# Kernel optimization log

Measured on AMD Instinct MI355X. Metric: run time of the kernel, lower is better.

The kernel has to match this reference:

```python
import jax, jax.numpy as jnp
import numpy as np

N = 10000      # nodes
E = 160000     # edges
C = 72         # hidden dim = 18 * mul (mul=4)
A = 16         # node_attr dim (16x0e)
L = 3          # layers
O = 64         # output dim (64x0e)
B = 16         # graphs in batch
IN_DIM = 18    # irreps_node_input dim
SH = 9         # spherical harmonics dim, lmax=2
FC = 100       # radial MLP hidden (fc_neurons=[1,100])
MAX_RADIUS = 2.0
NUM_NEIGHBORS = 16.0
NUM_NODES = 625.0


def sph_harm_l2(d):
    # component-normalized real spherical harmonics up to l=2 on unit vectors d [E,3]
    x, y, z = d[:, 0], d[:, 1], d[:, 2]
    s3, s5, s15 = 3.0 ** 0.5, 5.0 ** 0.5, 15.0 ** 0.5
    return jnp.stack([
        jnp.ones_like(x),
        s3 * x, s3 * y, s3 * z,
        s15 * x * y, s15 * y * z, (s5 / 2.0) * (3.0 * z * z - 1.0),
        s15 * x * z, (s15 / 2.0) * (x * x - y * y),
    ], axis=1)  # [E, 9]


def setup_inputs() -> dict:
    key = jax.random.key(0)
    ks = jax.random.split(key, 16)
    pos = jax.random.normal(ks[0], (N, 3), dtype=jnp.float32)
    node_attr = jax.random.normal(ks[1], (N, A), dtype=jnp.float32)
    batch = jnp.sort(jax.random.randint(ks[2], (N,), 0, B))
    edge_src = jax.random.randint(ks[3], (E,), 0, N)
    edge_dst = jax.random.randint(ks[4], (E,), 0, N)
    W_in = jax.random.normal(ks[5], (IN_DIM, C), dtype=jnp.float32) / np.sqrt(IN_DIM)
    W_tp = jax.random.normal(ks[6], (L, SH, C, C), dtype=jnp.float32) / np.sqrt(C)
    W_self = jax.random.normal(ks[7], (L, C, C), dtype=jnp.float32) / np.sqrt(C)
    W_attr = jax.random.normal(ks[8], (L, A, C), dtype=jnp.float32) / np.sqrt(A)
    fc1_w = jax.random.normal(ks[9], (L, 1, FC), dtype=jnp.float32)
    fc1_b = jnp.zeros((L, FC), dtype=jnp.float32)
    fc2_w = jax.random.normal(ks[10], (L, FC, SH), dtype=jnp.float32) / np.sqrt(FC)
    W_out = jax.random.normal(ks[11], (C, O), dtype=jnp.float32) / np.sqrt(C)
    return {"pos": pos, "node_attr": node_attr, "batch": batch,
            "edge_src": edge_src, "edge_dst": edge_dst,
            "W_in": W_in, "W_tp": W_tp, "W_self": W_self, "W_attr": W_attr,
            "fc1_w": fc1_w, "fc1_b": fc1_b, "fc2_w": fc2_w, "W_out": W_out}


def reference(pos, node_attr, batch, edge_src, edge_dst,
              W_in, W_tp, W_self, W_attr, fc1_w, fc1_b, fc2_w, W_out):
    n = pos.shape[0]
    # edge geometry
    rvec = pos[edge_src] - pos[edge_dst]                      # [E,3]
    r = jnp.linalg.norm(rvec, axis=1, keepdims=True)          # [E,1]
    dvec = rvec / jnp.maximum(r, 1e-9)
    sh = sph_harm_l2(dvec)                                    # [E,9]
    # single cosine radial basis with cutoff at max_radius (number_of_basis=1)
    t = r / MAX_RADIUS
    emb = jnp.where(t < 1.0, jnp.cos(0.5 * jnp.pi * t), 0.0)  # [E,1]
    # node inputs: fixed one-hot on the scalar channel, embedded to hidden dim
    onehot = jnp.zeros((IN_DIM,), dtype=pos.dtype).at[0].set(1.0)
    h = jnp.broadcast_to((onehot @ W_in)[None, :], (n, C))    # [N,C]
    for l in range(L):
        # radial MLP -> per-edge, per-SH-path weights
        u = jax.nn.silu(emb @ fc1_w[l] + fc1_b[l]) @ fc2_w[l]  # [E,9]
        path = u * sh                                          # [E,9]
        hs = h[edge_src]                                       # [E,C]
        m = jnp.zeros_like(hs)
        for s in range(SH):  # fixed small set of tensor-product paths
            m = m + path[:, s:s + 1] * (hs @ W_tp[l, s])       # [E,C]
        agg = jax.ops.segment_sum(m, edge_dst, num_segments=n) / np.sqrt(NUM_NEIGHBORS)
        h = jax.nn.gelu(agg + h @ W_self[l] + node_attr @ W_attr[l])
    out_nodes = h @ W_out                                      # [N,O]
    pooled = jax.ops.segment_sum(out_nodes, batch, num_segments=B)
    return pooled / np.sqrt(NUM_NODES)                         # [B,O]
```

## Files before the change

### kernel.cpp

```cpp
#include <hip/hip_runtime.h>
#include <math.h>

#define NN 10000
#define NE 160000
#define CC 72
#define AA 16
#define LL 3
#define OO 64
#define NBATCH 16
#define SH 9
#define FCN 100
#define KK (SH*CC)
#define KA 736
#define KP 768
#define KG 96
#define NT 5
#define PSTRIDE 12
#define NB 1024

typedef __attribute__((ext_vector_type(8))) short bf16x8;
typedef __attribute__((ext_vector_type(4))) float f32x4;

static __device__ __forceinline__ float gelu_tanh(float x) {
    float x3 = x * x * x;
    float inner = 0.7978845608028654f * (x + 0.044715f * x3);
    return 0.5f * x * (1.0f + tanhf(inner));
}
static __device__ __forceinline__ unsigned short f2bf(float x) {
    unsigned int u = __float_as_uint(x);
    u += 0x7FFFu + ((u >> 16) & 1u);
    return (unsigned short)(u >> 16);
}

__global__ void k_hist(const float* __restrict__ pos, const int* __restrict__ esrc,
                       const int* __restrict__ edst, int* __restrict__ cnt) {
    int e = blockIdx.x * blockDim.x + threadIdx.x;
    if (e >= NE) return;
    int s = esrc[e], d = edst[e];
    float dx = pos[3 * s] - pos[3 * d];
    float dy = pos[3 * s + 1] - pos[3 * d + 1];
    float dz = pos[3 * s + 2] - pos[3 * d + 2];
    float r = sqrtf(dx * dx + dy * dy + dz * dz);
    if (r * 0.5f < 1.0f) atomicAdd(&cnt[d], 1);
}

__global__ void k_scan(const int* __restrict__ cnt, int* __restrict__ off) {
    __shared__ int sa[256], sb[256];
    const int PER = 40;
    int t = threadIdx.x;
    int base = t * PER;
    int loc[PER];
    int run = 0;
#pragma unroll
    for (int i = 0; i < PER; ++i) {
        int idx = base + i;
        int v = (idx < NN) ? cnt[idx] : 0;
        loc[i] = run;
        run += v;
    }
    sa[t] = run;
    __syncthreads();
    int* in = sa; int* out = sb;
    for (int o = 1; o < 256; o <<= 1) {
        int v = in[t];
        if (t >= o) v += in[t - o];
        out[t] = v;
        __syncthreads();
        int* tmp = in; in = out; out = tmp;
    }
    int ebase = (t > 0) ? in[t - 1] : 0;
#pragma unroll
    for (int i = 0; i < PER; ++i) {
        int idx = base + i;
        if (idx <= NN) off[idx] = ebase + loc[i];
    }
}

__global__ void k_scatter2(const float* __restrict__ pos, const int* __restrict__ esrc,
                           const int* __restrict__ edst, const int* __restrict__ off,
                           int* __restrict__ cur, int* __restrict__ src_s,
                           int* __restrict__ dst_s) {
    int e = blockIdx.x * blockDim.x + threadIdx.x;
    if (e >= NE) return;
    int s = esrc[e], d = edst[e];
    float dx = pos[3 * s] - pos[3 * d];
    float dy = pos[3 * s + 1] - pos[3 * d + 1];
    float dz = pos[3 * s + 2] - pos[3 * d + 2];
    float r = sqrtf(dx * dx + dy * dy + dz * dz);
    if (r * 0.5f < 1.0f) {
        int slot = off[d] + atomicAdd(&cur[d], 1);
        src_s[slot] = s;
        dst_s[slot] = d;
    }
}

__global__ void k_utab(const float* __restrict__ fc1w, const float* __restrict__ fc1b,
                       const float* __restrict__ fc2w, float* __restrict__ U) {
    int i = blockIdx.x * blockDim.x + threadIdx.x;
    if (i >= LL * (NB + 1)) return;
    int l = i / (NB + 1), b = i - l * (NB + 1);
    float emb = cosf(1.5707963267948966f * ((float)b / (float)NB));
    float u[SH];
#pragma unroll
    for (int q = 0; q < SH; ++q) u[q] = 0.f;
    const float* w1 = &fc1w[l * FCN];
    const float* b1 = &fc1b[l * FCN];
    const float* w2 = &fc2w[l * FCN * SH];
    for (int f = 0; f < FCN; ++f) {
        float a = emb * w1[f] + b1[f];
        float si = a / (1.0f + expf(-a));
#pragma unroll
        for (int q = 0; q < SH; ++q) u[q] += si * w2[f * SH + q];
    }
    float* ud = &U[(size_t)i * 12];
#pragma unroll
    for (int q = 0; q < SH; ++q) ud[q] = u[q];
    ud[9] = 0.f; ud[10] = 0.f; ud[11] = 0.f;
}

__global__ __launch_bounds__(256) void k_path2(const float* __restrict__ pos,
                                               const int* __restrict__ src_s,
                                               const int* __restrict__ dst_s,
                                               const float* __restrict__ U,
                                               const int* __restrict__ off,
                                               float* __restrict__ path) {
    int slot = blockIdx.x * blockDim.x + threadIdx.x;
    if (slot >= off[NN]) return;
    int s = src_s[slot], d = dst_s[slot];
    float dx = pos[3 * s] - pos[3 * d];
    float dy = pos[3 * s + 1] - pos[3 * d + 1];
    float dz = pos[3 * s + 2] - pos[3 * d + 2];
    float r = sqrtf(dx * dx + dy * dy + dz * dz);
    float inv = 1.0f / fmaxf(r, 1e-9f);
    float x = dx * inv, y = dy * inv, z = dz * inv;
    const float s3 = 1.7320508075688772f;
    const float s5 = 2.23606797749979f;
    const float s15 = 3.872983346207417f;
    float sh[SH];
    sh[0] = 1.0f;
    sh[1] = s3 * x;
    sh[2] = s3 * y;
    sh[3] = s3 * z;
    sh[4] = s15 * x * y;
    sh[5] = s15 * y * z;
    sh[6] = 0.5f * s5 * (3.0f * z * z - 1.0f);
    sh[7] = s15 * x * z;
    sh[8] = 0.5f * s15 * (x * x - y * y);

    float fb = r * 0.5f * (float)NB;
    int b0 = (int)fb;
    float fr = fb - (float)b0;

#pragma unroll
    for (int l = 0; l < LL; ++l) {
        const float* t0 = &U[((size_t)l * (NB + 1) + b0) * 12];
        float4 a0 = *(const float4*)(t0 + 0);
        float4 a1 = *(const float4*)(t0 + 4);
        float  a2 = t0[8];
        float4 c0 = *(const float4*)(t0 + 12);
        float4 c1 = *(const float4*)(t0 + 16);
        float  c2 = t0[20];
        float u0 = a0.x + fr * (c0.x - a0.x);
        float u1 = a0.y + fr * (c0.y - a0.y);
        float u2 = a0.z + fr * (c0.z - a0.z);
        float u3 = a0.w + fr * (c0.w - a0.w);
        float u4 = a1.x + fr * (c1.x - a1.x);
        float u5 = a1.y + fr * (c1.y - a1.y);
        float u6 = a1.z + fr * (c1.z - a1.z);
        float u7 = a1.w + fr * (c1.w - a1.w);
        float u8 = a2   + fr * (c2   - a2);
        float* pd = &path[((size_t)l * NE + slot) * PSTRIDE];
        *(float4*)(pd + 0) = make_float4(u0 * sh[0], u1 * sh[1], u2 * sh[2], u3 * sh[3]);
        *(float4*)(pd + 4) = make_float4(u4 * sh[4], u5 * sh[5], u6 * sh[6], u7 * sh[7]);
        *(float4*)(pd + 8) = make_float4(u8 * sh[8], 0.f, 0.f, 0.f);
    }
}

__global__ void k_init(const float* __restrict__ W_in, float* __restrict__ h) {
    int i = blockIdx.x * blockDim.x + threadIdx.x;
    if (i < NN * CC) h[i] = W_in[i % CC];
}

__global__ void k_wcat2(const float* __restrict__ Wtp, const float* __restrict__ Wself,
                        const float* __restrict__ Wattr, unsigned short* __restrict__ Wb) {
    int i = blockIdx.x * blockDim.x + threadIdx.x;
    if (i >= LL * NT * KG * 128) return;
    int l = i / (NT * KG * 128);
    int rem = i - l * (NT * KG * 128);
    int nt = rem / (KG * 128); rem -= nt * (KG * 128);
    int kg = rem / 128; int e = rem - kg * 128;
    int n = nt * 16 + (e >> 3);
    int k = kg * 8 + (e & 7);
    float v = 0.f;
    if (n < CC && k < KA) {
        if (k < KK)            v = 0.25f * Wtp[(size_t)l * KK * CC + k * CC + n];
        else if (k < KK + CC)  v = Wself[(size_t)l * CC * CC + (k - KK) * CC + n];
        else                   v = Wattr[(size_t)l * AA * CC + (k - KK - CC) * CC + n];
    }
    Wb[i] = f2bf(v);
}

__global__ __launch_bounds__(1024) void k_layer(const float* __restrict__ h,
                                                const float* __restrict__ attr,
                                                const float* __restrict__ path_l,
                                                const int* __restrict__ src_s,
                                                const int* __restrict__ off,
                                                const unsigned short* __restrict__ Wb,
                                                float* __restrict__ hout) {
    __shared__ unsigned short Alds[KG * 128];
    __shared__ float red[3 * NT * 64 * 4];
    int t = threadIdx.x, w = t >> 6, lane = t & 63;
    int n0 = blockIdx.x * 16;
    int d = n0 + w;

    float a1[SH], a2[SH];
#pragma unroll
    for (int q = 0; q < SH; ++q) { a1[q] = 0.f; a2[q] = 0.f; }
    int b = off[d], e = off[d + 1];
    bool two = lane < (CC - 64);
    for (int i = b; i < e; ++i) {
        int s = src_s[i];
        float hv1 = h[(size_t)s * CC + lane];
        float hv2 = two ? h[(size_t)s * CC + 64 + lane] : 0.f;
        const float* p = &path_l[(size_t)i * PSTRIDE];
        float4 p0 = *(const float4*)p;
        float4 p1 = *(const float4*)(p + 4);
        float p8 = p[8];
        a1[0] += p0.x * hv1; a2[0] += p0.x * hv2;
        a1[1] += p0.y * hv1; a2[1] += p0.y * hv2;
        a1[2] += p0.z * hv1; a2[2] += p0.z * hv2;
        a1[3] += p0.w * hv1; a2[3] += p0.w * hv2;
        a1[4] += p1.x * hv1; a2[4] += p1.x * hv2;
        a1[5] += p1.y * hv1; a2[5] += p1.y * hv2;
        a1[6] += p1.z * hv1; a2[6] += p1.z * hv2;
        a1[7] += p1.w * hv1; a2[7] += p1.w * hv2;
        a1[8] += p8 * hv1;   a2[8] += p8 * hv2;
    }
    unsigned short* At = Alds + w * 8;
    int kgc = lane >> 3, kjc = lane & 7;
#pragma unroll
    for (int q = 0; q < SH; ++q) {
        At[(9 * q + kgc) * 128 + kjc] = f2bf(a1[q]);
        if (two) At[(9 * q + 8) * 128 + lane] = f2bf(a2[q]);
    }
    At[(81 + kgc) * 128 + kjc] = f2bf(h[(size_t)d * CC + lane]);
    if (two) At[89 * 128 + lane] = f2bf(h[(size_t)d * CC + 64 + lane]);
    if (lane < AA) At[(90 + (lane >> 3)) * 128 + (lane & 7)] = f2bf(attr[(size_t)d * AA + lane]);
    if (lane < 32) At[(92 + (lane >> 3)) * 128 + (lane & 7)] = 0;
    __syncthreads();

    if (w < 4) {
        const unsigned short* Ab = Alds + (lane & 15) * 8;
        const unsigned short* Bb = Wb + (lane & 15) * 8;
        f32x4 acc[NT];
#pragma unroll
        for (int nt = 0; nt < NT; ++nt) acc[nt] = (f32x4){0.f, 0.f, 0.f, 0.f};
        int s0 = w * 6;
#pragma unroll
        for (int s = 0; s < 6; ++s) {
            int kg = (s0 + s) * 4 + (lane >> 4);
            bf16x8 af = *(const bf16x8*)(Ab + (size_t)kg * 128);
#pragma unroll
            for (int nt = 0; nt < NT; ++nt) {
                bf16x8 bf = *(const bf16x8*)(Bb + ((size_t)nt * KG + kg) * 128);
                acc[nt] = __builtin_amdgcn_mfma_f32_16x16x32_bf16(af, bf, acc[nt], 0, 0, 0);
            }
        }
        if (w) {
#pragma unroll
            for (int nt = 0; nt < NT; ++nt)
                *(f32x4*)&red[(((w - 1) * NT + nt) * 64 + lane) * 4] = acc[nt];
        }
        __syncthreads();
        if (w == 0) {
            int cb = lane & 15, rb = (lane >> 4) * 4;
            int row = n0 + rb;
#pragma unroll
            for (int nt = 0; nt < NT; ++nt) {
                f32x4 p0 = *(const f32x4*)&red[((0 * NT + nt) * 64 + lane) * 4];
                f32x4 p1 = *(const f32x4*)&red[((1 * NT + nt) * 64 + lane) * 4];
                f32x4 p2 = *(const f32x4*)&red[((2 * NT + nt) * 64 + lane) * 4];
                int col = nt * 16 + cb;
                if (col < CC) {
#pragma unroll
                    for (int j = 0; j < 4; ++j) {
                        float v = acc[nt][j] + p0[j] + p1[j] + p2[j];
                        hout[(size_t)(row + j) * CC + col] = gelu_tanh(v);
                    }
                }
            }
        }
    } else {
        __syncthreads();
    }
}

__global__ __launch_bounds__(256) void k_pool(const float* __restrict__ h,
                                              const int* __restrict__ batch,
                                              float* __restrict__ hp) {
    __shared__ float sp[NBATCH * CC];
    int t = threadIdx.x;
    for (int i = t; i < NBATCH * CC; i += 256) sp[i] = 0.f;
    __syncthreads();
    int n0 = blockIdx.x * 16;
    for (int i = t; i < 16 * CC; i += 256) {
        int nl = i / CC, c = i - nl * CC;
        int n = n0 + nl;
        if (n < NN) atomicAdd(&sp[batch[n] * CC + c], h[(size_t)n * CC + c]);
    }
    __syncthreads();
    for (int i = t; i < NBATCH * CC; i += 256) {
        float v = sp[i];
        if (v != 0.f) atomicAdd(&hp[i], v);
    }
}

__global__ __launch_bounds__(1024) void k_outmm(const float* __restrict__ hp,
                                                const float* __restrict__ Wout,
                                                float* __restrict__ out) {
    __shared__ float hs[NBATCH * CC];
    int t = threadIdx.x;
    for (int i = t; i < NBATCH * CC; i += 1024) hs[i] = hp[i];
    __syncthreads();
    int b = t >> 6, o = t & 63;
    float acc = 0.f;
#pragma unroll 8
    for (int c = 0; c < CC; ++c) acc += hs[b * CC + c] * Wout[c * OO + o];
    out[t] = acc * (1.0f / 25.0f);
}

extern "C" void kernel_launch(void* const* d_in, const int* in_sizes, int n_in,
                              void* d_out, int out_size, void* d_ws, size_t ws_size,
                              hipStream_t stream) {
    const float* pos       = (const float*)d_in[0];
    const float* node_attr = (const float*)d_in[1];
    const int*   batch     = (const int*)d_in[2];
    const int*   esrc      = (const int*)d_in[3];
    const int*   edst      = (const int*)d_in[4];
    const float* W_in      = (const float*)d_in[5];
    const float* W_tp      = (const float*)d_in[6];
    const float* W_self    = (const float*)d_in[7];
    const float* W_attr    = (const float*)d_in[8];
    const float* fc1w      = (const float*)d_in[9];
    const float* fc1b      = (const float*)d_in[10];
    const float* fc2w      = (const float*)d_in[11];
    const float* W_out     = (const float*)d_in[12];
    float* out = (float*)d_out;

    char* p = (char*)d_ws;
    auto alloc = [&](size_t bytes) -> void* {
        void* r = (void*)p;
        p += (bytes + 255) & ~(size_t)255;
        return r;
    };
    int*   cnt   = (int*)alloc((size_t)NN * 4);
    int*   cur   = (int*)alloc((size_t)NN * 4);
    int*   off   = (int*)alloc((size_t)(NN + 1) * 4);
    int*   src_s = (int*)alloc((size_t)NE * 4);
    int*   dst_s = (int*)alloc((size_t)NE * 4);
    float* path  = (float*)alloc((size_t)LL * NE * PSTRIDE * 4);
    float* U     = (float*)alloc((size_t)LL * (NB + 1) * 12 * 4);
    unsigned short* Wb = (unsigned short*)alloc((size_t)LL * NT * KG * 128 * 2);
    float* h0    = (float*)alloc((size_t)NN * CC * 4);
    float* h1    = (float*)alloc((size_t)NN * CC * 4);
    float* hp    = (float*)alloc((size_t)NBATCH * CC * 4);

    hipMemsetAsync(cnt, 0, (size_t)NN * 4, stream);
    hipMemsetAsync(cur, 0, (size_t)NN * 4, stream);
    hipMemsetAsync(hp, 0, (size_t)NBATCH * CC * 4, stream);

    k_hist<<<(NE + 255) / 256, 256, 0, stream>>>(pos, esrc, edst, cnt);
    k_utab<<<(LL * (NB + 1) + 255) / 256, 256, 0, stream>>>(fc1w, fc1b, fc2w, U);
    k_wcat2<<<(LL * NT * KG * 128 + 255) / 256, 256, 0, stream>>>(W_tp, W_self, W_attr, Wb);
    k_init<<<(NN * CC + 255) / 256, 256, 0, stream>>>(W_in, h0);
    k_scan<<<1, 256, 0, stream>>>(cnt, off);
    k_scatter2<<<(NE + 255) / 256, 256, 0, stream>>>(pos, esrc, edst, off, cur, src_s, dst_s);
    k_path2<<<(NE + 255) / 256, 256, 0, stream>>>(pos, src_s, dst_s, U, off, path);

    const float* hin = h0;
    float* hout = h1;
    for (int l = 0; l < LL; ++l) {
        k_layer<<<NN / 16, 1024, 0, stream>>>(hin, node_attr,
                                              path + (size_t)l * NE * PSTRIDE, src_s, off,
                                              Wb + (size_t)l * NT * KG * 128, hout);
        const float* tmp = hin; hin = hout; hout = (float*)tmp;
    }
    k_pool<<<(NN + 15) / 16, 256, 0, stream>>>(hin, batch, hp);
    k_outmm<<<1, 1024, 0, stream>>>(hp, W_out, out);
}
```

Measured before the change: 166.0 us.

## Fuse prep kernels, store hidden state in bf16, stage path in LDS, split MFMA by tile

Four setup kernels (histogram, radial table, weight packing, h init) are merged into one launch, and the three memsets are collapsed into one by reordering the workspace. Hidden features are stored as bf16 to halve the gather traffic in each layer. Per-block path coefficients are staged in shared memory with batched source loads. The MFMA stage now assigns one output tile per wave instead of splitting K across waves and reducing through LDS. The bf16 hidden state loses precision across layers, and the EMAX chunk loop adds extra block barriers.

Result: faster. 150.8 us (-9.2%).

```diff
diff --git a/kernel.cpp b/kernel.cpp
--- a/kernel.cpp
+++ b/kernel.cpp
@@ -17,6 +17,7 @@
 #define NT 5
 #define PSTRIDE 12
 #define NB 1024
+#define EMAX 176
 
 typedef __attribute__((ext_vector_type(8))) short bf16x8;
 typedef __attribute__((ext_vector_type(4))) float f32x4;
@@ -31,17 +32,93 @@
     u += 0x7FFFu + ((u >> 16) & 1u);
     return (unsigned short)(u >> 16);
 }
-
-__global__ void k_hist(const float* __restrict__ pos, const int* __restrict__ esrc,
-                       const int* __restrict__ edst, int* __restrict__ cnt) {
-    int e = blockIdx.x * blockDim.x + threadIdx.x;
-    if (e >= NE) return;
-    int s = esrc[e], d = edst[e];
-    float dx = pos[3 * s] - pos[3 * d];
-    float dy = pos[3 * s + 1] - pos[3 * d + 1];
-    float dz = pos[3 * s + 2] - pos[3 * d + 2];
-    float r = sqrtf(dx * dx + dy * dy + dz * dz);
-    if (r * 0.5f < 1.0f) atomicAdd(&cnt[d], 1);
+static __device__ __forceinline__ float bf2f(unsigned short u) {
+    return __uint_as_float((unsigned int)u << 16);
+}
+
+#define GB_HIST 625
+#define GB_UTAB 13
+#define GB_WCAT 180
+#define GB_INIT 704
+#define GB_PREP (GB_HIST + GB_UTAB + GB_WCAT + GB_INIT)
+
+__global__ __launch_bounds__(256) void k_prep(
+        const float* __restrict__ pos, const int* __restrict__ esrc,
+        const int* __restrict__ edst, int* __restrict__ cnt,
+        const float* __restrict__ fc1w, const float* __restrict__ fc1b,
+        const float* __restrict__ fc2w, float* __restrict__ U,
+        const float* __restrict__ Wtp, const float* __restrict__ Wself,
+        const float* __restrict__ Wattr, unsigned short* __restrict__ Wb,
+        const float* __restrict__ W_in, unsigned short* __restrict__ h0) {
+    int bb = blockIdx.x, t = threadIdx.x;
+    if (bb < GB_HIST) {
+        int e = bb * 256 + t;
+        if (e < NE) {
+            int s = esrc[e], d = edst[e];
+            float dx = pos[3 * s] - pos[3 * d];
+            float dy = pos[3 * s + 1] - pos[3 * d + 1];
+            float dz = pos[3 * s + 2] - pos[3 * d + 2];
+            float r = sqrtf(dx * dx + dy * dy + dz * dz);
+            if (r * 0.5f < 1.0f) atomicAdd(&cnt[d], 1);
+        }
+        return;
+    }
+    bb -= GB_HIST;
+    if (bb < GB_UTAB) {
+        int i = bb * 256 + t;
+        if (i < LL * (NB + 1)) {
+            int l = i / (NB + 1), b = i - l * (NB + 1);
+            float emb = cosf(1.5707963267948966f * ((float)b / (float)NB));
+            float u[SH];
+#pragma unroll
+            for (int q = 0; q < SH; ++q) u[q] = 0.f;
+            const float* w1 = &fc1w[l * FCN];
+            const float* b1 = &fc1b[l * FCN];
+            const float* w2 = &fc2w[l * FCN * SH];
+            for (int f = 0; f < FCN; ++f) {
+                float a = emb * w1[f] + b1[f];
+                float si = a / (1.0f + expf(-a));
+#pragma unroll
+                for (int q = 0; q < SH; ++q) u[q] += si * w2[f * SH + q];
+            }
+            float* ud = &U[(size_t)i * 12];
+#pragma unroll
+            for (int q = 0; q < SH; ++q) ud[q] = u[q];
+            ud[9] = 0.f; ud[10] = 0.f; ud[11] = 0.f;
+        }
+        return;
+    }
+    bb -= GB_UTAB;
+    if (bb < GB_WCAT) {
+        int i0 = (bb * 256 + t) * 4;
+#pragma unroll
+        for (int u = 0; u < 4; ++u) {
+            int i = i0 + u;
+            int l = i / (NT * KG * 128);
+            int rem = i - l * (NT * KG * 128);
+            int nt = rem / (KG * 128); rem -= nt * (KG * 128);
+            int kg = rem / 128; int e = rem - kg * 128;
+            int n = nt * 16 + (e >> 3);
+            int k = kg * 8 + (e & 7);
+            float v = 0.f;
+            if (n < CC && k < KA) {
+                if (k < KK)            v = 0.25f * Wtp[(size_t)l * KK * CC + k * CC + n];
+                else if (k < KK + CC)  v = Wself[(size_t)l * CC * CC + (k - KK) * CC + n];
+                else                   v = Wattr[(size_t)l * AA * CC + (k - KK - CC) * CC + n];
+            }
+            Wb[i] = f2bf(v);
+        }
+        return;
+    }
+    bb -= GB_WCAT;
+    {
+        int i0 = (bb * 256 + t) * 4;
+#pragma unroll
+        for (int u = 0; u < 4; ++u) {
+            int i = i0 + u;
+            if (i < NN * CC) h0[i] = f2bf(W_in[i % CC]);
+        }
+    }
 }
 
 __global__ void k_scan(const int* __restrict__ cnt, int* __restrict__ off) {
@@ -92,30 +169,6 @@
         src_s[slot] = s;
         dst_s[slot] = d;
     }
-}
-
-__global__ void k_utab(const float* __restrict__ fc1w, const float* __restrict__ fc1b,
-                       const float* __restrict__ fc2w, float* __restrict__ U) {
-    int i = blockIdx.x * blockDim.x + threadIdx.x;
-    if (i >= LL * (NB + 1)) return;
-    int l = i / (NB + 1), b = i - l * (NB + 1);
-    float emb = cosf(1.5707963267948966f * ((float)b / (float)NB));
-    float u[SH];
-#pragma unroll
-    for (int q = 0; q < SH; ++q) u[q] = 0.f;
-    const float* w1 = &fc1w[l * FCN];
-    const float* b1 = &fc1b[l * FCN];
-    const float* w2 = &fc2w[l * FCN * SH];
-    for (int f = 0; f < FCN; ++f) {
-        float a = emb * w1[f] + b1[f];
-        float si = a / (1.0f + expf(-a));
-#pragma unroll
-        for (int q = 0; q < SH; ++q) u[q] += si * w2[f * SH + q];
-    }
-    float* ud = &U[(size_t)i * 12];
-#pragma unroll
-    for (int q = 0; q < SH; ++q) ud[q] = u[q];
-    ud[9] = 0.f; ud[10] = 0.f; ud[11] = 0.f;
 }
 
 __global__ __launch_bounds__(256) void k_path2(const float* __restrict__ pos,
@@ -176,66 +229,69 @@
     }
 }
 
-__global__ void k_init(const float* __restrict__ W_in, float* __restrict__ h) {
-    int i = blockIdx.x * blockDim.x + threadIdx.x;
-    if (i < NN * CC) h[i] = W_in[i % CC];
-}
-
-__global__ void k_wcat2(const float* __restrict__ Wtp, const float* __restrict__ Wself,
-                        const float* __restrict__ Wattr, unsigned short* __restrict__ Wb) {
-    int i = blockIdx.x * blockDim.x + threadIdx.x;
-    if (i >= LL * NT * KG * 128) return;
-    int l = i / (NT * KG * 128);
-    int rem = i - l * (NT * KG * 128);
-    int nt = rem / (KG * 128); rem -= nt * (KG * 128);
-    int kg = rem / 128; int e = rem - kg * 128;
-    int n = nt * 16 + (e >> 3);
-    int k = kg * 8 + (e & 7);
-    float v = 0.f;
-    if (n < CC && k < KA) {
-        if (k < KK)            v = 0.25f * Wtp[(size_t)l * KK * CC + k * CC + n];
-        else if (k < KK + CC)  v = Wself[(size_t)l * CC * CC + (k - KK) * CC + n];
-        else                   v = Wattr[(size_t)l * AA * CC + (k - KK - CC) * CC + n];
-    }
-    Wb[i] = f2bf(v);
-}
-
-__global__ __launch_bounds__(1024) void k_layer(const float* __restrict__ h,
-                                                const float* __restrict__ attr,
-                                                const float* __restrict__ path_l,
-                                                const int* __restrict__ src_s,
-                                                const int* __restrict__ off,
-                                                const unsigned short* __restrict__ Wb,
-                                                float* __restrict__ hout) {
+__global__ __launch_bounds__(1024, 8) void k_layer(
+        const unsigned short* __restrict__ h,
+        const float* __restrict__ attr,
+        const float* __restrict__ path_l,
+        const int* __restrict__ src_s,
+        const int* __restrict__ off,
+        const unsigned short* __restrict__ Wb,
+        unsigned short* __restrict__ hout) {
+    __shared__ float Plds[EMAX * PSTRIDE];
     __shared__ unsigned short Alds[KG * 128];
-    __shared__ float red[3 * NT * 64 * 4];
     int t = threadIdx.x, w = t >> 6, lane = t & 63;
     int n0 = blockIdx.x * 16;
     int d = n0 + w;
+    int b0 = off[n0], e0 = off[n0 + 16];
+    int db = off[d], de = off[d + 1];
 
     float a1[SH], a2[SH];
 #pragma unroll
     for (int q = 0; q < SH; ++q) { a1[q] = 0.f; a2[q] = 0.f; }
-    int b = off[d], e = off[d + 1];
     bool two = lane < (CC - 64);
-    for (int i = b; i < e; ++i) {
-        int s = src_s[i];
-        float hv1 = h[(size_t)s * CC + lane];
-        float hv2 = two ? h[(size_t)s * CC + 64 + lane] : 0.f;
-        const float* p = &path_l[(size_t)i * PSTRIDE];
-        float4 p0 = *(const float4*)p;
-        float4 p1 = *(const float4*)(p + 4);
-        float p8 = p[8];
-        a1[0] += p0.x * hv1; a2[0] += p0.x * hv2;
-        a1[1] += p0.y * hv1; a2[1] += p0.y * hv2;
-        a1[2] += p0.z * hv1; a2[2] += p0.z * hv2;
-        a1[3] += p0.w * hv1; a2[3] += p0.w * hv2;
-        a1[4] += p1.x * hv1; a2[4] += p1.x * hv2;
-        a1[5] += p1.y * hv1; a2[5] += p1.y * hv2;
-        a1[6] += p1.z * hv1; a2[6] += p1.z * hv2;
-        a1[7] += p1.w * hv1; a2[7] += p1.w * hv2;
-        a1[8] += p8 * hv1;   a2[8] += p8 * hv2;
-    }
+
+    for (int base = b0; base < e0; base += EMAX) {
+        int nE = min(EMAX, e0 - base);
+        const float4* p4 = (const float4*)(path_l + (size_t)base * PSTRIDE);
+        for (int idx = t; idx < nE * 3; idx += 1024)
+            *(float4*)&Plds[idx * 4] = p4[idx];
+        __syncthreads();
+        int lb = db > base ? db : base;
+        int le = de < base + nE ? de : base + nE;
+        for (int i = lb; i < le; i += 4) {
+            int m = le - i;
+            float h1v[4], h2v[4];
+#pragma unroll
+            for (int j = 0; j < 4; ++j) {
+                if (j < m) {
+                    int s = src_s[i + j];
+                    h1v[j] = bf2f(h[(size_t)s * CC + lane]);
+                    h2v[j] = two ? bf2f(h[(size_t)s * CC + 64 + lane]) : 0.f;
+                }
+            }
+#pragma unroll
+            for (int j = 0; j < 4; ++j) {
+                if (j < m) {
+                    const float* p = &Plds[(i + j - base) * PSTRIDE];
+                    float4 p0 = *(const float4*)p;
+                    float4 p1 = *(const float4*)(p + 4);
+                    float p8 = p[8];
+                    float hv1 = h1v[j], hv2 = h2v[j];
+                    a1[0] += p0.x * hv1; a2[0] += p0.x * hv2;
+                    a1[1] += p0.y * hv1; a2[1] += p0.y * hv2;
+                    a1[2] += p0.z * hv1; a2[2] += p0.z * hv2;
+                    a1[3] += p0.w * hv1; a2[3] += p0.w * hv2;
+                    a1[4] += p1.x * hv1; a2[4] += p1.x * hv2;
+                    a1[5] += p1.y * hv1; a2[5] += p1.y * hv2;
+                    a1[6] += p1.z * hv1; a2[6] += p1.z * hv2;
+                    a1[7] += p1.w * hv1; a2[7] += p1.w * hv2;
+                    a1[8] += p8 * hv1;   a2[8] += p8 * hv2;
+                }
+            }
+        }
+        __syncthreads();
+    }
+
     unsigned short* At = Alds + w * 8;
     int kgc = lane >> 3, kjc = lane & 7;
 #pragma unroll
@@ -243,59 +299,34 @@
         At[(9 * q + kgc) * 128 + kjc] = f2bf(a1[q]);
         if (two) At[(9 * q + 8) * 128 + lane] = f2bf(a2[q]);
     }
-    At[(81 + kgc) * 128 + kjc] = f2bf(h[(size_t)d * CC + lane]);
-    if (two) At[89 * 128 + lane] = f2bf(h[(size_t)d * CC + 64 + lane]);
+    At[(81 + kgc) * 128 + kjc] = h[(size_t)d * CC + lane];
+    if (two) At[89 * 128 + lane] = h[(size_t)d * CC + 64 + lane];
     if (lane < AA) At[(90 + (lane >> 3)) * 128 + (lane & 7)] = f2bf(attr[(size_t)d * AA + lane]);
     if (lane < 32) At[(92 + (lane >> 3)) * 128 + (lane & 7)] = 0;
     __syncthreads();
 
-    if (w < 4) {
+    if (w < NT) {
         const unsigned short* Ab = Alds + (lane & 15) * 8;
-        const unsigned short* Bb = Wb + (lane & 15) * 8;
-        f32x4 acc[NT];
-#pragma unroll
-        for (int nt = 0; nt < NT; ++nt) acc[nt] = (f32x4){0.f, 0.f, 0.f, 0.f};
-        int s0 = w * 6;
-#pragma unroll
-        for (int s = 0; s < 6; ++s) {
-            int kg = (s0 + s) * 4 + (lane >> 4);
+        const unsigned short* Bb = Wb + ((size_t)w * KG) * 128 + (lane & 15) * 8;
+        f32x4 acc = (f32x4){0.f, 0.f, 0.f, 0.f};
+#pragma unroll
+        for (int s = 0; s < 24; ++s) {
+            int kg = s * 4 + (lane >> 4);
             bf16x8 af = *(const bf16x8*)(Ab + (size_t)kg * 128);
-#pragma unroll
-            for (int nt = 0; nt < NT; ++nt) {
-                bf16x8 bf = *(const bf16x8*)(Bb + ((size_t)nt * KG + kg) * 128);
-                acc[nt] = __builtin_amdgcn_mfma_f32_16x16x32_bf16(af, bf, acc[nt], 0, 0, 0);
-            }
-        }
-        if (w) {
-#pragma unroll
-            for (int nt = 0; nt < NT; ++nt)
-                *(f32x4*)&red[(((w - 1) * NT + nt) * 64 + lane) * 4] = acc[nt];
-        }
-        __syncthreads();
-        if (w == 0) {
-            int cb = lane & 15, rb = (lane >> 4) * 4;
-            int row = n0 + rb;
-#pragma unroll
-            for (int nt = 0; nt < NT; ++nt) {
-                f32x4 p0 = *(const f32x4*)&red[((0 * NT + nt) * 64 + lane) * 4];
-                f32x4 p1 = *(const f32x4*)&red[((1 * NT + nt) * 64 + lane) * 4];
-                f32x4 p2 = *(const f32x4*)&red[((2 * NT + nt) * 64 + lane) * 4];
-                int col = nt * 16 + cb;
-                if (col < CC) {
-#pragma unroll
-                    for (int j = 0; j < 4; ++j) {
-                        float v = acc[nt][j] + p0[j] + p1[j] + p2[j];
-                        hout[(size_t)(row + j) * CC + col] = gelu_tanh(v);
-                    }
-                }
-            }
-        }
-    } else {
-        __syncthreads();
-    }
-}
-
-__global__ __launch_bounds__(256) void k_pool(const float* __restrict__ h,
+            bf16x8 bq = *(const bf16x8*)(Bb + (size_t)kg * 128);
+            acc = __builtin_amdgcn_mfma_f32_16x16x32_bf16(af, bq, acc, 0, 0, 0);
+        }
+        int cb = lane & 15, rb = (lane >> 4) * 4;
+        int row = n0 + rb, col = w * 16 + cb;
+        if (col < CC) {
+#pragma unroll
+            for (int j = 0; j < 4; ++j)
+                hout[(size_t)(row + j) * CC + col] = f2bf(gelu_tanh(acc[j]));
+        }
+    }
+}
+
+__global__ __launch_bounds__(256) void k_pool(const unsigned short* __restrict__ h,
                                               const int* __restrict__ batch,
                                               float* __restrict__ hp) {
     __shared__ float sp[NBATCH * CC];
@@ -306,7 +337,7 @@
     for (int i = t; i < 16 * CC; i += 256) {
         int nl = i / CC, c = i - nl * CC;
         int n = n0 + nl;
-        if (n < NN) atomicAdd(&sp[batch[n] * CC + c], h[(size_t)n * CC + c]);
+        if (n < NN) atomicAdd(&sp[batch[n] * CC + c], bf2f(h[(size_t)n * CC + c]));
     }
     __syncthreads();
     for (int i = t; i < NBATCH * CC; i += 256) {
@@ -353,37 +384,34 @@
         p += (bytes + 255) & ~(size_t)255;
         return r;
     };
+    size_t cntPad = ((size_t)NN * 4 + 255) & ~(size_t)255;
     int*   cnt   = (int*)alloc((size_t)NN * 4);
     int*   cur   = (int*)alloc((size_t)NN * 4);
+    float* hp    = (float*)alloc((size_t)NBATCH * CC * 4);
     int*   off   = (int*)alloc((size_t)(NN + 1) * 4);
     int*   src_s = (int*)alloc((size_t)NE * 4);
     int*   dst_s = (int*)alloc((size_t)NE * 4);
     float* path  = (float*)alloc((size_t)LL * NE * PSTRIDE * 4);
     float* U     = (float*)alloc((size_t)LL * (NB + 1) * 12 * 4);
     unsigned short* Wb = (unsigned short*)alloc((size_t)LL * NT * KG * 128 * 2);
-    float* h0    = (float*)alloc((size_t)NN * CC * 4);
-    float* h1    = (float*)alloc((size_t)NN * CC * 4);
-    float* hp    = (float*)alloc((size_t)NBATCH * CC * 4);
-
-    hipMemsetAsync(cnt, 0, (size_t)NN * 4, stream);
-    hipMemsetAsync(cur, 0, (size_t)NN * 4, stream);
-    hipMemsetAsync(hp, 0, (size_t)NBATCH * CC * 4, stream);
-
-    k_hist<<<(NE + 255) / 256, 256, 0, stream>>>(pos, esrc, edst, cnt);
-    k_utab<<<(LL * (NB + 1) + 255) / 256, 256, 0, stream>>>(fc1w, fc1b, fc2w, U);
-    k_wcat2<<<(LL * NT * KG * 128 + 255) / 256, 256, 0, stream>>>(W_tp, W_self, W_attr, Wb);
-    k_init<<<(NN * CC + 255) / 256, 256, 0, stream>>>(W_in, h0);
+    unsigned short* h0 = (unsigned short*)alloc((size_t)NN * CC * 2);
+    unsigned short* h1 = (unsigned short*)alloc((size_t)NN * CC * 2);
+
+    hipMemsetAsync(cnt, 0, cntPad * 2 + (size_t)NBATCH * CC * 4, stream);
+
+    k_prep<<<GB_PREP, 256, 0, stream>>>(pos, esrc, edst, cnt, fc1w, fc1b, fc2w, U,
+                                        W_tp, W_self, W_attr, Wb, W_in, h0);
     k_scan<<<1, 256, 0, stream>>>(cnt, off);
     k_scatter2<<<(NE + 255) / 256, 256, 0, stream>>>(pos, esrc, edst, off, cur, src_s, dst_s);
     k_path2<<<(NE + 255) / 256, 256, 0, stream>>>(pos, src_s, dst_s, U, off, path);
 
-    const float* hin = h0;
-    float* hout = h1;
+    const unsigned short* hin = h0;
+    unsigned short* hout = h1;
     for (int l = 0; l < LL; ++l) {
         k_layer<<<NN / 16, 1024, 0, stream>>>(hin, node_attr,
                                               path + (size_t)l * NE * PSTRIDE, src_s, off,
                                               Wb + (size_t)l * NT * KG * 128, hout);
-        const float* tmp = hin; hin = hout; hout = (float*)tmp;
+        const unsigned short* tmp = hin; hin = hout; hout = (unsigned short*)tmp;
     }
     k_pool<<<(NN + 15) / 16, 256, 0, stream>>>(hin, batch, hp);
     k_outmm<<<1, 1024, 0, stream>>>(hp, W_out, out);
```
